# Performance work log

Measured on AMD Instinct MI355X. Metric: run time of the kernel, lower is better.

## Reference

```python
import jax, jax.numpy as jnp
import numpy as np

N_NODES = 50000
N_EDGES = 400000
N_GRAPHS = 64
D_IN = 200
D_HID = 32
N_CLASS = 2


def setup_inputs() -> dict:
    key = jax.random.key(0)
    ks = jax.random.split(key, 16)
    x = jax.random.normal(ks[0], (N_NODES, D_IN), dtype=jnp.float32)
    edge_index = jax.random.randint(ks[1], (2, N_EDGES), 0, N_NODES, dtype=jnp.int64)
    edge_attr = jax.random.normal(ks[2], (N_EDGES,), dtype=jnp.float32)
    batch = jnp.sort(jax.random.randint(ks[3], (N_NODES,), 0, N_GRAPHS, dtype=jnp.int64))
    s = 0.05
    params = dict(
        W1r=jax.random.normal(ks[4], (D_IN, D_HID), jnp.float32) * s,
        W1l=jax.random.normal(ks[5], (D_IN, D_HID), jnp.float32) * s,
        b1=jnp.zeros((D_HID,), jnp.float32),
        W2r=jax.random.normal(ks[6], (D_HID, D_HID), jnp.float32) * s,
        W2l=jax.random.normal(ks[7], (D_HID, D_HID), jnp.float32) * s,
        b2=jnp.zeros((D_HID,), jnp.float32),
        W3r=jax.random.normal(ks[8], (D_HID, D_HID), jnp.float32) * s,
        W3l=jax.random.normal(ks[9], (D_HID, D_HID), jnp.float32) * s,
        b3=jnp.zeros((D_HID,), jnp.float32),
        Wlin=jax.random.normal(ks[10], (D_HID, N_CLASS), jnp.float32) * s,
        blin=jnp.zeros((N_CLASS,), jnp.float32),
    )
    return dict(x=x, edge_index=edge_index, edge_attr=edge_attr, batch=batch, **params)


def _graph_conv(x, src, dst, Wr, Wl, b):
    # PyG GraphConv: out_i = lin_rel(sum_{j->i} x_j) + lin_root(x_i)
    agg = jax.ops.segment_sum(x[src], dst, num_segments=x.shape[0])  # [N, d_in]
    return agg @ Wr + b + x @ Wl


def reference(x, edge_index, edge_attr, batch,
              W1r, W1l, b1, W2r, W2l, b2, W3r, W3l, b3, Wlin, blin):
    src, dst = edge_index[0], edge_index[1]
    # dropout is identity at inference (training=False)
    h = jax.nn.elu(_graph_conv(x, src, dst, W1r, W1l, b1))
    h = jax.nn.elu(_graph_conv(h, src, dst, W2r, W2l, b2))
    h = jax.nn.elu(_graph_conv(h, src, dst, W3r, W3l, b3))
    # global mean pool over graphs
    sums = jax.ops.segment_sum(h, batch, num_segments=N_GRAPHS)  # [G, d]
    counts = jax.ops.segment_sum(jnp.ones((h.shape[0],), h.dtype), batch,
                                 num_segments=N_GRAPHS)
    pooled = sums / jnp.maximum(counts, 1.0)[:, None]
    logits = pooled @ Wlin + blin
    return jax.nn.log_softmax(logits, axis=1)
```

## Files before the change

### kernel.cpp

```cpp
#include <hip/hip_runtime.h>
#include <hip/hip_bf16.h>


#define D_IN 200
#define N_GRAPHS 64

#define KP 232
#define KB 7
#define WT_ELEMS (64 * KP)
#define W23_ELEMS 2048
#define MAXDEG 32

#define NT 256
#define HS_STR 40

typedef __attribute__((ext_vector_type(8))) short bf16x8;
typedef __attribute__((ext_vector_type(4))) float f32x4;

__device__ __forceinline__ float4 elu4(float4 v) {
    float4 o;
    o.x = (v.x > 0.f) ? v.x : expm1f(v.x);
    o.y = (v.y > 0.f) ? v.y : expm1f(v.y);
    o.z = (v.z > 0.f) ? v.z : expm1f(v.z);
    o.w = (v.w > 0.f) ? v.w : expm1f(v.w);
    return o;
}

__global__ __launch_bounds__(NT) void count_pack(const int* __restrict__ src,
                                                 const int* __restrict__ dst,
                                                 int* __restrict__ cnt,
                                                 unsigned short* __restrict__ colIdx,
                                                 int E, int N,
                                                 const float* __restrict__ W1r,
                                                 const float* __restrict__ W1l,
                                                 const float* __restrict__ W2r,
                                                 const float* __restrict__ W2l,
                                                 const float* __restrict__ W3r,
                                                 const float* __restrict__ W3l,
                                                 __hip_bfloat16* __restrict__ Wt,
                                                 __hip_bfloat16* __restrict__ Wt2,
                                                 __hip_bfloat16* __restrict__ Wt3,
                                                 const int* __restrict__ batch,
                                                 int* __restrict__ starts,
                                                 int* __restrict__ ends,
                                                 int egrid, int wgrid, int w23g) {
    int blk = blockIdx.x;
    if (blk < egrid) {
        int e = blk * NT + threadIdx.x;
        if (e < E) {
            int d = dst[e];
            int r = atomicAdd(&cnt[d], 1);
            if (r < MAXDEG)
                colIdx[(long)r * N + d] = (unsigned short)src[e];
        }
    } else if (blk < egrid + wgrid) {
        int idx = (blk - egrid) * NT + threadIdx.x;
        if (idx < WT_ELEMS) {
            int n = idx / KP, k = idx % KP;
            float v = 0.f;
            if (k < D_IN) v = (n < 32) ? W1r[k * 32 + n] : W1l[k * 32 + (n - 32)];
            Wt[idx] = __float2bfloat16(v);
        }
    } else if (blk < egrid + wgrid + w23g) {
        int idx = (blk - egrid - wgrid) * NT + threadIdx.x;
        if (idx < 2 * W23_ELEMS) {
            int which = idx >> 11;
            int j = idx & 2047;
            int n = j >> 5, k = j & 31;
            const float* Wr = which ? W3r : W2r;
            const float* Wl = which ? W3l : W2l;
            float v = (n < 32) ? Wr[k * 32 + n] : Wl[k * 32 + (n - 32)];
            (which ? Wt3 : Wt2)[j] = __float2bfloat16(v);
        }
    } else {
        int i = (blk - egrid - wgrid - w23g) * NT + threadIdx.x;
        if (i < N) {
            int g = batch[i];
            if (i == 0 || batch[i - 1] != g) starts[g] = i;
            if (i == N - 1 || batch[i + 1] != g) ends[g] = i + 1;
        }
    }
}

__global__ __launch_bounds__(NT) void gemm1(const float* __restrict__ X,
                                            const __hip_bfloat16* __restrict__ Wt,
                                            __hip_bfloat16* __restrict__ yr16,
                                            __hip_bfloat16* __restrict__ ylb,
                                            int N) {
    __shared__ __hip_bfloat16 xs[64 * KP];
    int tid = threadIdx.x;
    long base = (long)blockIdx.x * 64;
    for (int s = tid; s < 64 * 58; s += NT) {
        int row = s / 58, pos = (s - row * 58) * 4;
        long grow = base + row;
        grow = (grow < (long)N) ? grow : (long)(N - 1);
        union { __hip_bfloat16 h[4]; uint2 v; } u;
        if (pos < D_IN) {
            float4 xv = *(const float4*)(X + grow * D_IN + pos);
            u.h[0] = __float2bfloat16(xv.x); u.h[1] = __float2bfloat16(xv.y);
            u.h[2] = __float2bfloat16(xv.z); u.h[3] = __float2bfloat16(xv.w);
        } else {
            u.v = make_uint2(0u, 0u);
        }
        *(uint2*)(&xs[row * KP + pos]) = u.v;
    }
    __syncthreads();

    int lane = tid & 63, wv = tid >> 6;
    int l15 = lane & 15, q = lane >> 4;
    bf16x8 a[KB];
#pragma unroll
    for (int kb = 0; kb < KB; ++kb)
        a[kb] = *(const bf16x8*)(const void*)
            (&xs[(wv * 16 + l15) * KP + kb * 32 + q * 8]);
#pragma unroll
    for (int ns = 0; ns < 4; ++ns) {
        f32x4 acc = {0.f, 0.f, 0.f, 0.f};
#pragma unroll
        for (int kb = 0; kb < KB; ++kb) {
            bf16x8 bfrag = *(const bf16x8*)(const void*)
                (Wt + (ns * 16 + l15) * KP + kb * 32 + q * 8);
            acc = __builtin_amdgcn_mfma_f32_16x16x32_bf16(a[kb], bfrag, acc, 0, 0, 0);
        }
        int col = ns * 16 + l15;
#pragma unroll
        for (int r = 0; r < 4; ++r) {
            long node = base + wv * 16 + q * 4 + r;
            if (node < N) {
                if (col < 32) yr16[node * 32 + col] = __float2bfloat16(acc[r]);
                else          ylb[node * 32 + (col - 32)] = __float2bfloat16(acc[r]);
            }
        }
    }
}

__device__ __forceinline__ void agg_node8(const __hip_bfloat16* __restrict__ yr16,
                                          const __hip_bfloat16* __restrict__ ylb,
                                          const int* __restrict__ cnt,
                                          const unsigned short* __restrict__ colIdx,
                                          const float* __restrict__ b,
                                          int node, int ln, int half, int N,
                                          float4& oA, float4& oB) {
    const uint4* yv = (const uint4*)yr16;
    int deg = cnt[node]; deg = (deg < MAXDEG) ? deg : MAXDEG;
    int f0 = ln * 8;
    float4 bA = *(const float4*)(b + f0);
    float4 bB = *(const float4*)(b + f0 + 4);
    uint4 rv = *(const uint4*)(ylb + (long)node * 32 + f0);
    float4 rA = make_float4(__uint_as_float(rv.x << 16),
                            __uint_as_float(rv.x & 0xffff0000u),
                            __uint_as_float(rv.y << 16),
                            __uint_as_float(rv.y & 0xffff0000u));
    float4 rB = make_float4(__uint_as_float(rv.z << 16),
                            __uint_as_float(rv.z & 0xffff0000u),
                            __uint_as_float(rv.w << 16),
                            __uint_as_float(rv.w & 0xffff0000u));
    float acc[8] = {0.f, 0.f, 0.f, 0.f, 0.f, 0.f, 0.f, 0.f};
    for (int p0 = half; p0 < deg; p0 += 16) {
        int jj[8]; float m[8];
#pragma unroll
        for (int i = 0; i < 8; ++i) {
            int pi = p0 + 2 * i;
            m[i] = (pi < deg) ? 1.f : 0.f;
            pi = (pi < deg) ? pi : (deg - 1);
            jj[i] = (int)colIdx[(long)pi * N + node];
        }
        uint4 v[8];
#pragma unroll
        for (int i = 0; i < 8; ++i) v[i] = yv[(long)jj[i] * 4 + ln];
#pragma unroll
        for (int i = 0; i < 8; ++i) {
            uint d0 = v[i].x, d1 = v[i].y, d2 = v[i].z, d3 = v[i].w;
            acc[0] = fmaf(__uint_as_float(d0 << 16),          m[i], acc[0]);
            acc[1] = fmaf(__uint_as_float(d0 & 0xffff0000u),  m[i], acc[1]);
            acc[2] = fmaf(__uint_as_float(d1 << 16),          m[i], acc[2]);
            acc[3] = fmaf(__uint_as_float(d1 & 0xffff0000u),  m[i], acc[3]);
            acc[4] = fmaf(__uint_as_float(d2 << 16),          m[i], acc[4]);
            acc[5] = fmaf(__uint_as_float(d2 & 0xffff0000u),  m[i], acc[5]);
            acc[6] = fmaf(__uint_as_float(d3 << 16),          m[i], acc[6]);
            acc[7] = fmaf(__uint_as_float(d3 & 0xffff0000u),  m[i], acc[7]);
        }
    }
#pragma unroll
    for (int t = 0; t < 8; ++t) acc[t] += __shfl_xor(acc[t], 4);
    oA = elu4(make_float4(acc[0] + bA.x + rA.x, acc[1] + bA.y + rA.y,
                          acc[2] + bA.z + rA.z, acc[3] + bA.w + rA.w));
    oB = elu4(make_float4(acc[4] + bB.x + rB.x, acc[5] + bB.y + rB.y,
                          acc[6] + bB.z + rB.z, acc[7] + bB.w + rB.w));
}

template<int LAYER>
__global__ __launch_bounds__(NT) void agg_gemm_mfma(
        const __hip_bfloat16* __restrict__ yr16_in,
        const __hip_bfloat16* __restrict__ ylb_in,
        const int* __restrict__ cnt, const unsigned short* __restrict__ colIdx,
        const float* __restrict__ b, const __hip_bfloat16* __restrict__ Wt2,
        __hip_bfloat16* __restrict__ yr16_out,
        __hip_bfloat16* __restrict__ ylb_out, int N) {
    __shared__ __hip_bfloat16 hs[32 * HS_STR];
    int tid = threadIdx.x;
    int ln = tid & 3, half = (tid >> 2) & 1, nl = tid >> 3;
    long base = (long)blockIdx.x * 32;
    int node = (int)base + nl;
    int nodec = (node < N) ? node : (N - 1);
    float4 oA, oB;
    agg_node8(yr16_in, ylb_in, cnt, colIdx, b, nodec, ln, half, N, oA, oB);
    union { __hip_bfloat16 h[8]; float4 v; } u;
    if (node < N) {
        u.h[0] = __float2bfloat16(oA.x); u.h[1] = __float2bfloat16(oA.y);
        u.h[2] = __float2bfloat16(oA.z); u.h[3] = __float2bfloat16(oA.w);
        u.h[4] = __float2bfloat16(oB.x); u.h[5] = __float2bfloat16(oB.y);
        u.h[6] = __float2bfloat16(oB.z); u.h[7] = __float2bfloat16(oB.w);
    } else {
        u.v = make_float4(0.f, 0.f, 0.f, 0.f);
    }
    if (half == 0)
        *(float4*)(&hs[nl * HS_STR + ln * 8]) = u.v;
    __syncthreads();

    int lane = tid & 63, w = tid >> 6;
    int l15 = lane & 15, q = lane >> 4;
    int rg = w & 1, cg = w >> 1;
    bf16x8 a = *(const bf16x8*)(const void*)(&hs[(rg * 16 + l15) * HS_STR + q * 8]);
#pragma unroll
    for (int s = 0; s < 2; ++s) {
        int ns = cg * 2 + s;
        f32x4 acc = {0.f, 0.f, 0.f, 0.f};
        bf16x8 bfrag = *(const bf16x8*)(const void*)(Wt2 + (ns * 16 + l15) * 32 + q * 8);
        acc = __builtin_amdgcn_mfma_f32_16x16x32_bf16(a, bfrag, acc, 0, 0, 0);
        int col = ns * 16 + l15;
#pragma unroll
        for (int r = 0; r < 4; ++r) {
            long nd = base + rg * 16 + q * 4 + r;
            if (nd < N) {
                if (col < 32) yr16_out[nd * 32 + col] = __float2bfloat16(acc[r]);
                else          ylb_out[nd * 32 + (col - 32)] = __float2bfloat16(acc[r]);
            }
        }
    }
}

__global__ __launch_bounds__(NT) void agg_elu_k(const __hip_bfloat16* __restrict__ yr16,
                                                const __hip_bfloat16* __restrict__ ylb,
                                                const int* __restrict__ cnt,
                                                const unsigned short* __restrict__ colIdx,
                                                const float* __restrict__ b,
                                                float* __restrict__ hout, int N) {
    int tid = threadIdx.x;
    int ln = tid & 3, half = (tid >> 2) & 1;
    int node = blockIdx.x * 32 + (tid >> 3);
    int nodec = (node < N) ? node : (N - 1);
    float4 oA, oB;
    agg_node8(yr16, ylb, cnt, colIdx, b, nodec, ln, half, N, oA, oB);
    if (half == 0 && node < N) {
        int f0 = ln * 8;
        *(float4*)(hout + (long)node * 32 + f0) = oA;
        *(float4*)(hout + (long)node * 32 + f0 + 4) = oB;
    }
}

__global__ __launch_bounds__(NT) void pool_head(const float4* __restrict__ h4,
                                                const int* __restrict__ starts,
                                                const int* __restrict__ ends,
                                                const float* __restrict__ Wlin,
                                                const float* __restrict__ blin,
                                                float* __restrict__ out, int N) {
    int g = blockIdx.x;
    int start = starts[g];
    int end = ends[g];

    int f4 = threadIdx.x & 7, r = threadIdx.x >> 3;
    float4 acc = make_float4(0.f, 0.f, 0.f, 0.f);
    for (int i = start + r; i < end; i += 32) {
        float4 v = h4[(long)i * 8 + f4];
        acc.x += v.x; acc.y += v.y; acc.z += v.z; acc.w += v.w;
    }
    __shared__ float4 red[32][8];
    __shared__ float pooledS[32];
    red[r][f4] = acc;
    __syncthreads();
    if (r == 0) {
        float4 s = make_float4(0.f, 0.f, 0.f, 0.f);
#pragma unroll
        for (int r2 = 0; r2 < 32; ++r2) {
            float4 v = red[r2][f4];
            s.x += v.x; s.y += v.y; s.z += v.z; s.w += v.w;
        }
        float inv = 1.f / fmaxf((float)(end - start), 1.f);
        pooledS[f4 * 4 + 0] = s.x * inv;
        pooledS[f4 * 4 + 1] = s.y * inv;
        pooledS[f4 * 4 + 2] = s.z * inv;
        pooledS[f4 * 4 + 3] = s.w * inv;
    }
    __syncthreads();
    if (threadIdx.x == 0) {
        float c0 = blin[0], c1 = blin[1];
        for (int k = 0; k < 32; ++k) {
            float pk = pooledS[k];
            c0 += pk * Wlin[k * 2 + 0];
            c1 += pk * Wlin[k * 2 + 1];
        }
        float m = fmaxf(c0, c1);
        float lse = m + logf(expf(c0 - m) + expf(c1 - m));
        out[g * 2 + 0] = c0 - lse;
        out[g * 2 + 1] = c1 - lse;
    }
}

extern "C" void kernel_launch(void* const* d_in, const int* in_sizes, int n_in,
                              void* d_out, int out_size, void* d_ws, size_t ws_size,
                              hipStream_t stream) {
    const float* x     = (const float*)d_in[0];
    const int*   eidx  = (const int*)d_in[1];
    const int*   batch = (const int*)d_in[3];
    const float* W1r = (const float*)d_in[4];
    const float* W1l = (const float*)d_in[5];
    const float* b1  = (const float*)d_in[6];
    const float* W2r = (const float*)d_in[7];
    const float* W2l = (const float*)d_in[8];
    const float* b2  = (const float*)d_in[9];
    const float* W3r = (const float*)d_in[10];
    const float* W3l = (const float*)d_in[11];
    const float* b3  = (const float*)d_in[12];
    const float* Wlin = (const float*)d_in[13];
    const float* blin = (const float*)d_in[14];
    float* out = (float*)d_out;

    const int N = in_sizes[0] / D_IN;
    const int E = in_sizes[1] / 2;
    const int* src = eidx;
    const int* dst = eidx + E;

    char* w = (char*)d_ws;
    auto alloc = [&](size_t bytes) -> void* {
        void* p = (void*)w;
        w += (bytes + 255) & ~(size_t)255;
        return p;
    };
    int* cnt    = (int*)alloc((size_t)(N + 128) * 4);
    int* starts = cnt + N;
    int* ends   = cnt + N + 64;
    unsigned short* colIdx = (unsigned short*)alloc((size_t)N * MAXDEG * 2);
    __hip_bfloat16* Wt    = (__hip_bfloat16*)alloc((size_t)WT_ELEMS * 2);
    __hip_bfloat16* Wt2   = (__hip_bfloat16*)alloc((size_t)W23_ELEMS * 2);
    __hip_bfloat16* Wt3   = (__hip_bfloat16*)alloc((size_t)W23_ELEMS * 2);
    __hip_bfloat16* yr16A = (__hip_bfloat16*)alloc((size_t)N * 32 * 2);
    __hip_bfloat16* yr16B = (__hip_bfloat16*)alloc((size_t)N * 32 * 2);
    __hip_bfloat16* ylA   = (__hip_bfloat16*)alloc((size_t)N * 32 * 2);
    __hip_bfloat16* ylB   = (__hip_bfloat16*)alloc((size_t)N * 32 * 2);
    float* hA  = (float*)alloc((size_t)N * 32 * 4);

    hipMemsetAsync(cnt, 0, (size_t)(N + 128) * 4, stream);

    int egrid = (E + NT - 1) / NT;
    int wgrid = (WT_ELEMS + NT - 1) / NT;
    int w23g  = (2 * W23_ELEMS + NT - 1) / NT;
    int ngrid = (N + NT - 1) / NT;
    int t64   = (N + 63) / 64;
    int g32   = (N + 31) / 32;

    count_pack<<<egrid + wgrid + w23g + ngrid, NT, 0, stream>>>(
        src, dst, cnt, colIdx, E, N, W1r, W1l, W2r, W2l, W3r, W3l,
        Wt, Wt2, Wt3, batch, starts, ends, egrid, wgrid, w23g);
    gemm1<<<t64, NT, 0, stream>>>(x, Wt, yr16A, ylA, N);
    agg_gemm_mfma<1><<<g32, NT, 0, stream>>>(yr16A, ylA, cnt, colIdx, b1, Wt2,
                                             yr16B, ylB, N);
    agg_gemm_mfma<2><<<g32, NT, 0, stream>>>(yr16B, ylB, cnt, colIdx, b2, Wt3,
                                             yr16A, ylA, N);
    agg_elu_k<<<g32, NT, 0, stream>>>(yr16A, ylA, cnt, colIdx, b3, hA, N);
    pool_head<<<N_GRAPHS, NT, 0, stream>>>((const float4*)hA, starts, ends,
                                           Wlin, blin, out, N);
}
```

Measured before the change: 176.6 us.

## Fuse final aggregation with mean-pool via shared and global atomics

```diff
diff --git a/kernel.cpp b/kernel.cpp
--- a/kernel.cpp
+++ b/kernel.cpp
@@ -240,63 +240,69 @@
     }
 }
 
-__global__ __launch_bounds__(NT) void agg_elu_k(const __hip_bfloat16* __restrict__ yr16,
-                                                const __hip_bfloat16* __restrict__ ylb,
-                                                const int* __restrict__ cnt,
-                                                const unsigned short* __restrict__ colIdx,
-                                                const float* __restrict__ b,
-                                                float* __restrict__ hout, int N) {
+__global__ __launch_bounds__(NT) void agg_pool(const __hip_bfloat16* __restrict__ yr16,
+                                               const __hip_bfloat16* __restrict__ ylb,
+                                               const int* __restrict__ cnt,
+                                               const unsigned short* __restrict__ colIdx,
+                                               const float* __restrict__ b,
+                                               const int* __restrict__ batch,
+                                               float* __restrict__ pooled, int N) {
+    __shared__ float ps[4][32];
     int tid = threadIdx.x;
     int ln = tid & 3, half = (tid >> 2) & 1;
-    int node = blockIdx.x * 32 + (tid >> 3);
+    long base = (long)blockIdx.x * 32;
+    int node = (int)base + (tid >> 3);
     int nodec = (node < N) ? node : (N - 1);
     float4 oA, oB;
     agg_node8(yr16, ylb, cnt, colIdx, b, nodec, ln, half, N, oA, oB);
+    if (tid < 128) ps[tid >> 5][tid & 31] = 0.f;
+    __syncthreads();
+    int g0 = batch[(int)base];
     if (half == 0 && node < N) {
+        int loc = batch[node] - g0;
         int f0 = ln * 8;
-        *(float4*)(hout + (long)node * 32 + f0) = oA;
-        *(float4*)(hout + (long)node * 32 + f0 + 4) = oB;
-    }
-}
-
-__global__ __launch_bounds__(NT) void pool_head(const float4* __restrict__ h4,
-                                                const int* __restrict__ starts,
-                                                const int* __restrict__ ends,
-                                                const float* __restrict__ Wlin,
-                                                const float* __restrict__ blin,
-                                                float* __restrict__ out, int N) {
+        if (loc < 4) {
+            atomicAdd(&ps[loc][f0 + 0], oA.x); atomicAdd(&ps[loc][f0 + 1], oA.y);
+            atomicAdd(&ps[loc][f0 + 2], oA.z); atomicAdd(&ps[loc][f0 + 3], oA.w);
+            atomicAdd(&ps[loc][f0 + 4], oB.x); atomicAdd(&ps[loc][f0 + 5], oB.y);
+            atomicAdd(&ps[loc][f0 + 6], oB.z); atomicAdd(&ps[loc][f0 + 7], oB.w);
+        } else {
+            int gb = (g0 + loc) * 32 + f0;
+            atomicAdd(&pooled[gb + 0], oA.x); atomicAdd(&pooled[gb + 1], oA.y);
+            atomicAdd(&pooled[gb + 2], oA.z); atomicAdd(&pooled[gb + 3], oA.w);
+            atomicAdd(&pooled[gb + 4], oB.x); atomicAdd(&pooled[gb + 5], oB.y);
+            atomicAdd(&pooled[gb + 6], oB.z); atomicAdd(&pooled[gb + 7], oB.w);
+        }
+    }
+    __syncthreads();
+    if (tid < 128) {
+        int slot = tid >> 5, feat = tid & 31;
+        int g = g0 + slot;
+        float v = ps[slot][feat];
+        if (v != 0.f && g < N_GRAPHS)
+            atomicAdd(&pooled[g * 32 + feat], v);
+    }
+}
+
+__global__ __launch_bounds__(64) void head(const float* __restrict__ pooled,
+                                           const int* __restrict__ starts,
+                                           const int* __restrict__ ends,
+                                           const float* __restrict__ Wlin,
+                                           const float* __restrict__ blin,
+                                           float* __restrict__ out) {
     int g = blockIdx.x;
-    int start = starts[g];
-    int end = ends[g];
-
-    int f4 = threadIdx.x & 7, r = threadIdx.x >> 3;
-    float4 acc = make_float4(0.f, 0.f, 0.f, 0.f);
-    for (int i = start + r; i < end; i += 32) {
-        float4 v = h4[(long)i * 8 + f4];
-        acc.x += v.x; acc.y += v.y; acc.z += v.z; acc.w += v.w;
-    }
-    __shared__ float4 red[32][8];
-    __shared__ float pooledS[32];
-    red[r][f4] = acc;
-    __syncthreads();
-    if (r == 0) {
-        float4 s = make_float4(0.f, 0.f, 0.f, 0.f);
-#pragma unroll
-        for (int r2 = 0; r2 < 32; ++r2) {
-            float4 v = red[r2][f4];
-            s.x += v.x; s.y += v.y; s.z += v.z; s.w += v.w;
-        }
-        float inv = 1.f / fmaxf((float)(end - start), 1.f);
-        pooledS[f4 * 4 + 0] = s.x * inv;
-        pooledS[f4 * 4 + 1] = s.y * inv;
-        pooledS[f4 * 4 + 2] = s.z * inv;
-        pooledS[f4 * 4 + 3] = s.w * inv;
-    }
-    __syncthreads();
-    if (threadIdx.x == 0) {
+    int t = threadIdx.x;
+    __shared__ float ph[32];
+    if (t < 32) {
+        float inv = 1.f / fmaxf((float)(ends[g] - starts[g]), 1.f);
+        ph[t] = pooled[g * 32 + t] * inv;
+    }
+    __syncthreads();
+    if (t == 0) {
         float c0 = blin[0], c1 = blin[1];
+#pragma unroll
         for (int k = 0; k < 32; ++k) {
-            float pk = pooledS[k];
+            float pk = ph[k];
             c0 += pk * Wlin[k * 2 + 0];
             c1 += pk * Wlin[k * 2 + 1];
         }
@@ -337,9 +343,10 @@
         w += (bytes + 255) & ~(size_t)255;
         return p;
     };
-    int* cnt    = (int*)alloc((size_t)(N + 128) * 4);
+    int* cnt    = (int*)alloc((size_t)(N + 128 + 2048) * 4);
     int* starts = cnt + N;
     int* ends   = cnt + N + 64;
+    float* pooled = (float*)(cnt + N + 128);
     unsigned short* colIdx = (unsigned short*)alloc((size_t)N * MAXDEG * 2);
     __hip_bfloat16* Wt    = (__hip_bfloat16*)alloc((size_t)WT_ELEMS * 2);
     __hip_bfloat16* Wt2   = (__hip_bfloat16*)alloc((size_t)W23_ELEMS * 2);
@@ -348,9 +355,8 @@
     __hip_bfloat16* yr16B = (__hip_bfloat16*)alloc((size_t)N * 32 * 2);
     __hip_bfloat16* ylA   = (__hip_bfloat16*)alloc((size_t)N * 32 * 2);
     __hip_bfloat16* ylB   = (__hip_bfloat16*)alloc((size_t)N * 32 * 2);
-    float* hA  = (float*)alloc((size_t)N * 32 * 4);
-
-    hipMemsetAsync(cnt, 0, (size_t)(N + 128) * 4, stream);
+
+    hipMemsetAsync(cnt, 0, (size_t)(N + 128 + 2048) * 4, stream);
 
     int egrid = (E + NT - 1) / NT;
     int wgrid = (WT_ELEMS + NT - 1) / NT;
@@ -367,7 +373,6 @@
                                              yr16B, ylB, N);
     agg_gemm_mfma<2><<<g32, NT, 0, stream>>>(yr16B, ylB, cnt, colIdx, b2, Wt3,
                                              yr16A, ylA, N);
-    agg_elu_k<<<g32, NT, 0, stream>>>(yr16A, ylA, cnt, colIdx, b3, hA, N);
-    pool_head<<<N_GRAPHS, NT, 0, stream>>>((const float4*)hA, starts, ends,
-                                           Wlin, blin, out, N);
-}
+    agg_pool<<<g32, NT, 0, stream>>>(yr16A, ylA, cnt, colIdx, b3, batch, pooled, N);
+    head<<<N_GRAPHS, 64, 0, stream>>>(pooled, starts, ends, Wlin, blin, out);
+}
```

After: 182.7 us. 1.03x slower.
